# Optimization experiments

Hardware: AMD Instinct MI355X
Metric: run time of the kernel (lower is better)

Reference implementation:

```python
import jax, jax.numpy as jnp
import numpy as np

N = 4096
DIM = 128      # dim_in
HID = 256      # mlp hidden_dim
K_IN = 8       # k for linear_k

def _knn_edges(dist, k):
    # dist: [n,n]; k nearest neighbors excluding self (matches heapq loop)
    n = dist.shape[0]
    d = jnp.where(jnp.eye(n, dtype=bool), jnp.inf, dist)
    nbr = jax.lax.top_k(-d, k)[1]                     # [n,k] indices of k smallest
    src = jnp.repeat(jnp.arange(n), k)                # res[0] = i
    dst = nbr.reshape(-1)                             # res[1] = neighbor
    return src, dst

def _gcn_conv(x, src, dst, W, b):
    # torch_geometric GCNConv: add self loops + symmetric normalization
    n = x.shape[0]
    loop = jnp.arange(n)
    s = jnp.concatenate([src, loop])
    t = jnp.concatenate([dst, loop])
    xw = x @ W
    deg = jax.ops.segment_sum(jnp.ones(s.shape[0], x.dtype), t, num_segments=n)
    dinv = jax.lax.rsqrt(deg)                         # deg >= 1 due to self loops
    norm = dinv[s] * dinv[t]
    out = jax.ops.segment_sum(norm[:, None] * xw[s], t, num_segments=n)
    return out + b

def _gcn(x, src, dst, Wg1, bg1, Wg2, bg2):
    h = jax.nn.relu(_gcn_conv(x, src, dst, Wg1, bg1))
    h = _gcn_conv(h, src, dst, Wg2, bg2)              # dropout is identity in eval
    return jax.nn.log_softmax(h, axis=1)

def _conv2d(x, w, b):
    y = jax.lax.conv_general_dilated(x, w, (1, 1), 'SAME',
        dimension_numbers=('NCHW', 'OIHW', 'NCHW'))
    return y + b.reshape(1, -1, 1, 1)

def setup_inputs():
    key = jax.random.key(0)
    ks = jax.random.split(key, 20)
    f32 = jnp.float32
    def w(k, shape):
        fan = shape[0]
        return (jax.random.uniform(k, shape, f32) * 2 - 1) * (1.0 / np.sqrt(fan))
    return {
        'data_x_1': jax.random.normal(ks[0], (1, N, 4), f32),
        'data_x_2': jax.random.normal(ks[1], (1, N, K_IN, 4), f32),
        'Wk': w(ks[2], (K_IN, 1)),        'bk': jnp.zeros((1,), f32),
        'Wg1': w(ks[3], (8, DIM // 2)),   'bg1': jnp.zeros((DIM // 2,), f32),
        'Wg2': w(ks[4], (DIM // 2, DIM)), 'bg2': jnp.zeros((DIM,), f32),
        'Wq': w(ks[5], (3 * DIM, DIM)),   'bq': jnp.zeros((DIM,), f32),
        'Wkey': w(ks[6], (3 * DIM, DIM)), 'bkey': jnp.zeros((DIM,), f32),
        'Woff': w(ks[7], (4, DIM)),       'boff': jnp.zeros((DIM,), f32),
        'pw': jnp.full((1,), 0.25, f32),
        'Wf1': w(ks[8], (DIM, HID)),      'bf1': jnp.zeros((HID,), f32),
        'Wf2': w(ks[9], (HID, HID)),      'bf2': jnp.zeros((HID,), f32),
        'Wf3': w(ks[10], (HID, 4)),       'bf3': jnp.zeros((4,), f32),
        'Wcy3': w(ks[11], (1, 1, 1, 3)),  'bcy3': jnp.zeros((1,), f32),
        'Wcx3': w(ks[12], (1, 1, 3, 1)),  'bcx3': jnp.zeros((1,), f32),
        'Wcy5': w(ks[13], (1, 1, 1, 5)),  'bcy5': jnp.zeros((1,), f32),
        'Wcx5': w(ks[14], (1, 1, 5, 1)),  'bcx5': jnp.zeros((1,), f32),
        'Wcy9': w(ks[15], (1, 1, 1, 9)),  'bcy9': jnp.zeros((1,), f32),
        'Wcx9': w(ks[16], (1, 1, 9, 1)),  'bcx9': jnp.zeros((1,), f32),
    }

def reference(data_x_1, data_x_2, Wk, bk, Wg1, bg1, Wg2, bg2, Wq, bq, Wkey, bkey,
              Woff, boff, pw, Wf1, bf1, Wf2, bf2, Wf3, bf3,
              Wcy3, bcy3, Wcx3, bcx3, Wcy5, bcy5, Wcx5, bcx5, Wcy9, bcy9, Wcx9, bcx9):
    # linear_k over k dimension: [1,n,k,4] -> transpose -> [1,n,4,k] -> [1,n,4]
    dx2 = jnp.swapaxes(data_x_2, 2, 3)
    dx2_out = (dx2 @ Wk + bk)[..., 0]
    data_x = jnp.concatenate([data_x_1, dx2_out], axis=2)   # [1,n,8]
    Ot = data_x[:, :, 4:]                                   # [1,n,4]

    pos = data_x[:, :, 0:2]
    diff = pos[:, :, None, :] - pos[:, None, :, :]          # [1,n,n,2]
    distances = jnp.linalg.norm(diff, axis=3)               # [1,n,n]
    maxd = jnp.max(distances, axis=2, keepdims=True)
    oushi_atte = 1.0 - distances / maxd                     # [1,n,n]

    x0 = data_x[0]
    dist0 = jax.lax.stop_gradient(distances[0])             # knn on detached dist
    embs = []
    for kk in (3, 5, 9):
        src, dst = _knn_edges(dist0, kk)
        embs.append(_gcn(x0, src, dst, Wg1, bg1, Wg2, bg2)[None])
    embedding = jnp.concatenate(embs, axis=2)               # [1,n,3*DIM]

    query = embedding @ Wq + bq                             # [1,n,DIM]
    key_t = embedding @ Wkey + bkey
    scores = jnp.einsum('bnd,bmd->bnm', query, key_t) / jnp.sqrt(jnp.float32(DIM))
    A = scores / jnp.max(scores, axis=2, keepdims=True)     # [1,n,n]

    A4 = A[None]                                            # [1,1,n,n]
    c3 = _conv2d(A4, Wcy3, bcy3) + _conv2d(A4, Wcx3, bcx3)
    c5 = _conv2d(A4, Wcy5, bcy5) + _conv2d(A4, Wcx5, bcx5)
    c9 = _conv2d(A4, Wcy9, bcy9) + _conv2d(A4, Wcx9, bcx9)

    A_cat = jnp.concatenate([A, oushi_atte, c3[0], c5[0], c9[0]], axis=2)  # [1,n,5n]
    A_cat = (A_cat - A_cat.min()) / (A_cat.max() - A_cat.min())

    Ot5 = jnp.tile(Ot, (1, 5, 1))                           # [1,5n,4]
    h = jnp.matmul(A_cat, Ot5)                              # [1,n,4]
    h = h @ Woff + boff                                     # [1,n,DIM]
    h = jnp.where(h > 0, h, pw * h)                         # PReLU (scalar weight)
    h = jax.nn.relu(h @ Wf1 + bf1)
    h = jax.nn.relu(h @ Wf2 + bf2)
    return h @ Wf3 + bf3                                    # [1,n,4]
```

## Files before the change

### kernel.cpp

```cpp
#include <hip/hip_runtime.h>
#include <math.h>

#define NN 4096

typedef __bf16 bf16x8 __attribute__((ext_vector_type(8)));
typedef float  f32x4  __attribute__((ext_vector_type(4)));

static __device__ __forceinline__ unsigned enc_f(float f){
    unsigned u = __float_as_uint(f);
    return (u & 0x80000000u) ? ~u : (u | 0x80000000u);
}
static __device__ __forceinline__ float dec_f(unsigned u){
    unsigned b = (u & 0x80000000u) ? (u & 0x7fffffffu) : ~u;
    return __uint_as_float(b);
}

__global__ void k_prep(const float* __restrict__ dx1, const float* __restrict__ dx2,
                       const float* __restrict__ Wk, const float* __restrict__ bk,
                       float* __restrict__ x0, float* __restrict__ colsum){
    int n = blockIdx.x*blockDim.x + threadIdx.x;
    if (n >= NN) return;
    float wk[8];
    #pragma unroll
    for (int j=0;j<8;j++) wk[j] = Wk[j];
    float bkv = bk[0];
    #pragma unroll
    for (int c=0;c<4;c++) x0[n*8+c] = dx1[n*4+c];
    #pragma unroll
    for (int c=0;c<4;c++){
        float acc = bkv;
        #pragma unroll
        for (int j=0;j<8;j++) acc += dx2[(n*8+j)*4+c]*wk[j];
        x0[n*8+4+c] = acc;
        atomicAdd(&colsum[c], acc);
    }
}

__global__ void k_ty(const float* __restrict__ x0,
        const float* __restrict__ Wcy3, const float* __restrict__ Wcy5, const float* __restrict__ Wcy9,
        float* __restrict__ Ty){
    int j = blockIdx.x*256 + threadIdx.x;
    if (j >= NN) return;
    float Cy[9];
    #pragma unroll
    for (int o=-4;o<=4;o++){
        float c = Wcy9[o+4];
        if (o>=-2 && o<=2) c += Wcy5[o+2];
        if (o>=-1 && o<=1) c += Wcy3[o+1];
        Cy[o+4] = c;
    }
    float4 acc = {0,0,0,0};
    #pragma unroll
    for (int o=-4;o<=4;o++){
        int jj = j - o;
        if ((unsigned)jj < NN){
            float4 ot = *(const float4*)&x0[jj*8+4];
            float c = Cy[o+4];
            acc.x += c*ot.x; acc.y += c*ot.y; acc.z += c*ot.z; acc.w += c*ot.w;
        }
    }
    *(float4*)&Ty[j*4] = acc;
}

__global__ __launch_bounds__(256) void k_dist(const float* __restrict__ dx1,
        const float* __restrict__ x0,
        float* __restrict__ maxd, int* __restrict__ nbr,
        int* __restrict__ cnt3, int* __restrict__ cnt5, int* __restrict__ cnt9,
        float* __restrict__ dOt){
    __shared__ float2 ps[NN];
    int tid = threadIdx.x;
    for (int j=tid; j<NN; j+=256){
        float4 v = *(const float4*)&dx1[j*4];
        ps[j] = make_float2(v.x, v.y);
    }
    __syncthreads();
    int lane = tid & 63;
    int i = blockIdx.x*4 + (tid>>6);
    float2 pi = ps[i];
    unsigned long long best[9];
    #pragma unroll
    for (int q=0;q<9;q++) best[q] = ~0ULL;
    float lmax = 0.f;
    float4 dacc = {0,0,0,0};
    for (int t=0;t<64;t++){
        int j = (t<<6) | lane;
        float2 p = ps[j];
        float dx = pi.x - p.x, dy = pi.y - p.y;
        float d = sqrtf(dx*dx + dy*dy);
        lmax = fmaxf(lmax, d);
        float4 otj = *(const float4*)&x0[j*8+4];
        dacc.x += d*otj.x; dacc.y += d*otj.y; dacc.z += d*otj.z; dacc.w += d*otj.w;
        unsigned long long cand = ((unsigned long long)__float_as_uint(d) << 32) | (unsigned)j;
        if (j != i && cand < best[8]){
            best[8] = cand;
            #pragma unroll
            for (int q=8; q>0; --q){
                if (best[q] < best[q-1]){ unsigned long long tm=best[q]; best[q]=best[q-1]; best[q-1]=tm; }
            }
        }
    }
    #pragma unroll
    for (int m=1;m<64;m<<=1){
        lmax = fmaxf(lmax, __shfl_xor(lmax, m, 64));
        dacc.x += __shfl_xor(dacc.x, m, 64);
        dacc.y += __shfl_xor(dacc.y, m, 64);
        dacc.z += __shfl_xor(dacc.z, m, 64);
        dacc.w += __shfl_xor(dacc.w, m, 64);
    }
    if (lane==0){
        maxd[i] = lmax;
        *(float4*)&dOt[i*4] = dacc;
    }
    for (int t=0;t<9;t++){
        unsigned long long w = best[0];
        #pragma unroll
        for (int m=1;m<64;m<<=1){
            unsigned long long o = __shfl_xor(w, m, 64);
            if (o < w) w = o;
        }
        if (best[0] == w){
            #pragma unroll
            for (int q=0;q<8;q++) best[q] = best[q+1];
            best[8] = ~0ULL;
        }
        if (lane==0){
            int j = (int)(w & 0xffffffffu);
            nbr[i*9+t] = j;
            atomicAdd(&cnt9[j], 1);
            if (t<5) atomicAdd(&cnt5[j], 1);
            if (t<3) atomicAdd(&cnt3[j], 1);
        }
    }
}

__global__ __launch_bounds__(256) void k_scan(const int* __restrict__ cnt3,
        const int* __restrict__ cnt5, const int* __restrict__ cnt9,
        int* __restrict__ offc, float* __restrict__ dinvc){
    __shared__ int part[256];
    int tid = threadIdx.x;
    for (int g=0; g<3; g++){
        const int* cp = g==0?cnt3:(g==1?cnt5:cnt9);
        int base = tid*16;
        int loc[16]; int s=0;
        #pragma unroll
        for (int q=0;q<16;q++){ loc[q]=s; s += cp[base+q]; }
        part[tid]=s; __syncthreads();
        for (int d=1; d<256; d<<=1){
            int v = (tid>=d) ? part[tid-d] : 0;
            __syncthreads();
            part[tid] += v;
            __syncthreads();
        }
        int pre = (tid==0) ? 0 : part[tid-1];
        #pragma unroll
        for (int q=0;q<16;q++){
            offc[g*NN + base + q]  = pre + loc[q];
            dinvc[g*NN + base + q] = rsqrtf((float)cp[base+q] + 1.f);
        }
        __syncthreads();
    }
}

__global__ void k_fill(const int* __restrict__ nbr, const int* __restrict__ offc,
        int* __restrict__ cur, int* __restrict__ rev){
    int i = blockIdx.x*256 + threadIdx.x;
    if (i >= NN) return;
    #pragma unroll
    for (int t=0;t<9;t++){
        int j = nbr[i*9+t];
        int gmin = t<3 ? 0 : (t<5 ? 1 : 2);
        for (int g=gmin; g<3; g++){
            int pos = atomicAdd(&cur[g*NN+j], 1);
            int rb = (g==0) ? 0 : (g==1 ? NN*3 : NN*8);
            rev[rb + offc[g*NN+j] + pos] = i;
        }
    }
}

__global__ void k_y1(const float* __restrict__ x0, const float* __restrict__ Wg1,
                     float* __restrict__ xw){
    int idx = blockIdx.x*256 + threadIdx.x;
    if (idx >= NN*64) return;
    int n = idx>>6, c = idx&63;
    float acc = 0.f;
    #pragma unroll
    for (int k=0;k<8;k++) acc += x0[n*8+k]*Wg1[k*64+c];
    xw[idx] = acc;
}

__global__ __launch_bounds__(256) void k_h1y2(const float* __restrict__ xw,
        const int* __restrict__ offc,
        const int* __restrict__ cnt3, const int* __restrict__ cnt5, const int* __restrict__ cnt9,
        const int* __restrict__ rev, const float* __restrict__ dinvc,
        const float* __restrict__ bg1, const float* __restrict__ Wg2,
        float* __restrict__ y2){
    __shared__ float h1s[12][64];
    int n0 = blockIdx.x*4, tid = threadIdx.x;
    for (int s=tid; s<768; s+=256){
        int p = s>>6, k = s&63, g = p>>2, n = n0+(p&3);
        const int* cp = g==0?cnt3:(g==1?cnt5:cnt9);
        int rb = (g==0) ? 0 : (g==1 ? NN*3 : NN*8);
        int cnt = cp[n];
        int o = rb + offc[g*NN+n];
        float dv = dinvc[g*NN+n];
        float srow = dv*xw[n*64+k];
        for (int e=0;e<cnt;e++){
            int i = rev[o+e];
            srow += dinvc[g*NN+i]*xw[i*64+k];
        }
        float v = dv*srow + bg1[k];
        h1s[p][k] = v>0.f ? v : 0.f;
    }
    __syncthreads();
    int c = tid & 127, ph = tid>>7;
    float a6[6] = {0,0,0,0,0,0};
    for (int k=0;k<64;k++){
        float w = Wg2[k*128+c];
        #pragma unroll
        for (int q=0;q<6;q++) a6[q] += h1s[q*2+ph][k]*w;
    }
    #pragma unroll
    for (int q=0;q<6;q++){
        int p = q*2+ph, g = p>>2, n = n0+(p&3);
        float dv = dinvc[g*NN+n];
        y2[(size_t)g*NN*128 + (size_t)n*128 + c] = dv*a6[q];
    }
}

__global__ __launch_bounds__(128) void k_fin(const float* __restrict__ y2,
        const int* __restrict__ offc,
        const int* __restrict__ cnt3, const int* __restrict__ cnt5, const int* __restrict__ cnt9,
        const int* __restrict__ rev, const float* __restrict__ dinvc,
        const float* __restrict__ bg2, float* __restrict__ emb){
    __shared__ float sm[2], ss[2];
    int b = blockIdx.x;
    int n = b & (NN-1), g = b >> 12;
    const int* cp = g==0?cnt3:(g==1?cnt5:cnt9);
    int rb = (g==0) ? 0 : (g==1 ? NN*3 : NN*8);
    int cnt = cp[n];
    int o = rb + offc[g*NN+n];
    float dv = dinvc[g*NN+n];
    int c = threadIdx.x;
    const float* yg = y2 + (size_t)g*NN*128;
    float s = yg[(size_t)n*128 + c];
    for (int e=0;e<cnt;e++){
        int i = rev[o+e];
        s += yg[(size_t)i*128 + c];
    }
    float v = dv*s + bg2[c];
    float m = v;
    #pragma unroll
    for (int st=1;st<64;st<<=1) m = fmaxf(m, __shfl_xor(m, st, 64));
    if ((c&63)==0) sm[c>>6] = m;
    __syncthreads();
    m = fmaxf(sm[0], sm[1]);
    float e = expf(v - m);
    float t = e;
    #pragma unroll
    for (int st=1;st<64;st<<=1) t += __shfl_xor(t, st, 64);
    if ((c&63)==0) ss[c>>6] = t;
    __syncthreads();
    t = ss[0]+ss[1];
    emb[n*384 + g*128 + c] = v - m - logf(t);
}

__global__ __launch_bounds__(256) void k_qk(const float* __restrict__ emb,
        const float* __restrict__ Wq, const float* __restrict__ bq,
        const float* __restrict__ Wkey, const float* __restrict__ bkey,
        __bf16* __restrict__ qh, __bf16* __restrict__ ql,
        __bf16* __restrict__ kh, __bf16* __restrict__ kl){
    __shared__ float es[8][384];
    int n0 = blockIdx.x*8;
    int tid = threadIdx.x;
    for (int idx=tid; idx<8*384; idx+=256){
        int m = idx/384, k = idx%384;
        es[m][k] = emb[(n0+m)*384+k];
    }
    __syncthreads();
    int c = tid & 127;
    int sel = tid >> 7;
    const float* W = sel ? Wkey : Wq;
    float b = sel ? bkey[c] : bq[c];
    float acc[8];
    #pragma unroll
    for (int m=0;m<8;m++) acc[m]=b;
    for (int k=0;k<384;k++){
        float w = W[k*128+c];
        #pragma unroll
        for (int m=0;m<8;m++) acc[m] += es[m][k]*w;
    }
    __bf16* oh = sel ? kh : qh;
    __bf16* ol = sel ? kl : ql;
    #pragma unroll
    for (int m=0;m<8;m++){
        float v = acc[m];
        __bf16 h = (__bf16)v;
        oh[(size_t)(n0+m)*128+c] = h;
        ol[(size_t)(n0+m)*128+c] = (__bf16)(v - (float)h);
    }
}

__global__ __launch_bounds__(256) void k_scores(
        const __bf16* __restrict__ qh, const __bf16* __restrict__ ql,
        const __bf16* __restrict__ kh, const __bf16* __restrict__ kl,
        float* __restrict__ scores,
        unsigned* __restrict__ rowmaxenc, unsigned* __restrict__ rowminenc){
    int bx = blockIdx.x & 31;
    int by = blockIdx.x >> 5;
    int tid = threadIdx.x;
    int w = tid >> 6, lane = tid & 63;
    int li = lane & 15, g = lane >> 4;
    int r0 = by*128 + (w>>1)*64;
    int c0 = bx*128 + (w&1)*64;

    f32x4 acc[4][4] = {};
    for (int ks=0; ks<4; ++ks){
        int kofs = ks*32 + g*8;
        bf16x8 ah[4], al[4], bh[4], bl[4];
        #pragma unroll
        for (int f=0; f<4; ++f){
            ah[f] = *(const bf16x8*)&qh[(size_t)(r0+f*16+li)*128 + kofs];
            al[f] = *(const bf16x8*)&ql[(size_t)(r0+f*16+li)*128 + kofs];
            bh[f] = *(const bf16x8*)&kh[(size_t)(c0+f*16+li)*128 + kofs];
            bl[f] = *(const bf16x8*)&kl[(size_t)(c0+f*16+li)*128 + kofs];
        }
        #pragma unroll
        for (int fr=0; fr<4; ++fr){
            #pragma unroll
            for (int fc=0; fc<4; ++fc){
                acc[fr][fc] = __builtin_amdgcn_mfma_f32_16x16x32_bf16(ah[fr], bh[fc], acc[fr][fc], 0, 0, 0);
                acc[fr][fc] = __builtin_amdgcn_mfma_f32_16x16x32_bf16(ah[fr], bl[fc], acc[fr][fc], 0, 0, 0);
                acc[fr][fc] = __builtin_amdgcn_mfma_f32_16x16x32_bf16(al[fr], bh[fc], acc[fr][fc], 0, 0, 0);
            }
        }
    }
    #pragma unroll
    for (int fr=0; fr<4; ++fr){
        #pragma unroll
        for (int r=0; r<4; ++r){
            int row = r0 + fr*16 + g*4 + r;
            float mx = -INFINITY, mn = INFINITY;
            #pragma unroll
            for (int fc=0; fc<4; ++fc){
                float v = acc[fr][fc][r];
                scores[(size_t)row*NN + c0 + fc*16 + li] = v;
                mx = fmaxf(mx, v);
                mn = fminf(mn, v);
            }
            #pragma unroll
            for (int s=1; s<16; s<<=1){
                mx = fmaxf(mx, __shfl_xor(mx, s, 64));
                mn = fminf(mn, __shfl_xor(mn, s, 64));
            }
            if (li == 0){
                atomicMax(&rowmaxenc[row], enc_f(mx));
                atomicMin(&rowminenc[row], enc_f(mn));
            }
        }
    }
}

__global__ __launch_bounds__(256) void k_cstream(const float* __restrict__ scores,
        const unsigned* __restrict__ rowmaxenc,
        const float* __restrict__ Wcy3, const float* __restrict__ Wcx3,
        const float* __restrict__ Wcy5, const float* __restrict__ Wcx5,
        const float* __restrict__ Wcy9, const float* __restrict__ Wcx9,
        const float* __restrict__ bcy3, const float* __restrict__ bcx3,
        const float* __restrict__ bcy5, const float* __restrict__ bcx5,
        const float* __restrict__ bcy9, const float* __restrict__ bcx9,
        float* __restrict__ mnmx){
    __shared__ float smn[4], smx[4];
    int tid = threadIdx.x;
    int w = tid >> 6, lane = tid & 63;
    int strip = blockIdx.x*4 + w;
    int jj = strip*56 - 4 + lane;
    bool cvalid = (unsigned)jj < NN;
    bool outLane = (lane >= 4) && (lane < 60) && cvalid;
    int i0 = blockIdx.y*64;

    float wy3[3],wx3[3],wy5[5],wx5[5],wy9[9],wx9[9];
    #pragma unroll
    for (int t=0;t<3;t++){ wy3[t]=Wcy3[t]; wx3[t]=Wcx3[t]; }
    #pragma unroll
    for (int t=0;t<5;t++){ wy5[t]=Wcy5[t]; wx5[t]=Wcx5[t]; }
    #pragma unroll
    for (int t=0;t<9;t++){ wy9[t]=Wcy9[t]; wx9[t]=Wcx9[t]; }
    float bc3 = bcy3[0]+bcx3[0];
    float bc5 = bcy5[0]+bcx5[0];
    float bc9 = bcy9[0]+bcx9[0];

    float win[9], cy3r[9], cy5r[9], cy9r[9];
    float mn = INFINITY, mx = -INFINITY;

    for (int tb = 0; tb < 8; ++tb){
        #pragma unroll
        for (int u = 0; u < 9; ++u){
            int t  = tb*9 + u;
            int ri = i0 - 4 + t;
            float a = 0.f;
            if (((unsigned)ri < NN) && cvalid)
                a = scores[(size_t)ri*NN + jj] * (1.f/dec_f(rowmaxenc[ri]));
            float tp[9];
            #pragma unroll
            for (int k=0;k<9;k++) tp[k] = (k==4) ? a : __shfl(a, lane + k - 4, 64);
            float cy9v = ((tp[0]*wy9[0] + tp[1]*wy9[1]) + (tp[2]*wy9[2] + tp[3]*wy9[3]))
                       + ((tp[4]*wy9[4] + tp[5]*wy9[5]) + (tp[6]*wy9[6] + tp[7]*wy9[7]))
                       + tp[8]*wy9[8];
            float cy5v = ((tp[2]*wy5[0] + tp[3]*wy5[1]) + (tp[4]*wy5[2] + tp[5]*wy5[3]))
                       + tp[6]*wy5[4];
            float cy3v = (tp[3]*wy3[0] + tp[4]*wy3[1]) + tp[5]*wy3[2];
            win[u]  = a;
            cy3r[u] = cy3v; cy5r[u] = cy5v; cy9r[u] = cy9v;
            if (t >= 8 && outLane){
                float cx9v = ((win[(u+1)%9]*wx9[0] + win[(u+2)%9]*wx9[1]) + (win[(u+3)%9]*wx9[2] + win[(u+4)%9]*wx9[3]))
                           + ((win[(u+5)%9]*wx9[4] + win[(u+6)%9]*wx9[5]) + (win[(u+7)%9]*wx9[6] + win[(u+8)%9]*wx9[7]))
                           + win[u]*wx9[8];
                float cx5v = ((win[(u+3)%9]*wx5[0] + win[(u+4)%9]*wx5[1]) + (win[(u+5)%9]*wx5[2] + win[(u+6)%9]*wx5[3]))
                           + win[(u+7)%9]*wx5[4];
                float cx3v = (win[(u+4)%9]*wx3[0] + win[(u+5)%9]*wx3[1]) + win[(u+6)%9]*wx3[2];
                float c9 = cy9r[(u+5)%9] + cx9v + bc9;
                float c5 = cy5r[(u+5)%9] + cx5v + bc5;
                float c3 = cy3r[(u+5)%9] + cx3v + bc3;
                mn = fminf(mn, fminf(fminf(c3,c5),c9));
                mx = fmaxf(mx, fmaxf(fmaxf(c3,c5),c9));
            }
        }
    }
    #pragma unroll
    for (int m=1; m<64; m<<=1){
        mn = fminf(mn, __shfl_xor(mn, m, 64));
        mx = fmaxf(mx, __shfl_xor(mx, m, 64));
    }
    if (lane == 0){ smn[w] = mn; smx[w] = mx; }
    __syncthreads();
    if (tid == 0){
        float a0 = fminf(fminf(smn[0],smn[1]), fminf(smn[2],smn[3]));
        float b0 = fmaxf(fmaxf(smx[0],smx[1]), fmaxf(smx[2],smx[3]));
        int bid = blockIdx.y*gridDim.x + blockIdx.x;
        mnmx[bid] = a0;
        mnmx[1216 + bid] = b0;
    }
}

__global__ __launch_bounds__(256) void k_rowdot(const float* __restrict__ scores,
        const float* __restrict__ x0, const float* __restrict__ Ty,
        const unsigned* __restrict__ rowmaxenc, const float* __restrict__ maxd,
        const float* __restrict__ dOt, const float* __restrict__ colsum,
        const float* __restrict__ bcy3, const float* __restrict__ bcx3,
        const float* __restrict__ bcy5, const float* __restrict__ bcx5,
        const float* __restrict__ bcy9, const float* __restrict__ bcx9,
        float* __restrict__ ASdot, float* __restrict__ Bv){
    int tid = threadIdx.x;
    int tc = tid & 31, tr = tid >> 5;
    int i = blockIdx.x*8 + tr;
    const float* srow = scores + (size_t)i*NN;
    float4 ss = {0,0,0,0}, st = {0,0,0,0};
    for (int c0 = tc; c0 < NN; c0 += 32){
        float sv = srow[c0];
        float4 ot = *(const float4*)&x0[c0*8+4];
        float4 ty = *(const float4*)&Ty[c0*4];
        ss.x += sv*ot.x; ss.y += sv*ot.y; ss.z += sv*ot.z; ss.w += sv*ot.w;
        st.x += sv*ty.x; st.y += sv*ty.y; st.z += sv*ty.z; st.w += sv*ty.w;
    }
    #pragma unroll
    for (int s=1; s<32; s<<=1){
        ss.x += __shfl_xor(ss.x, s, 64); ss.y += __shfl_xor(ss.y, s, 64);
        ss.z += __shfl_xor(ss.z, s, 64); ss.w += __shfl_xor(ss.w, s, 64);
        st.x += __shfl_xor(st.x, s, 64); st.y += __shfl_xor(st.y, s, 64);
        st.z += __shfl_xor(st.z, s, 64); st.w += __shfl_xor(st.w, s, 64);
    }
    if (tc == 0){
        float iv = 1.f/dec_f(rowmaxenc[i]);
        float imv = 1.f/maxd[i];
        float bcsum = bcy3[0]+bcx3[0]+bcy5[0]+bcx5[0]+bcy9[0]+bcx9[0];
        float4 cs = *(const float4*)colsum;
        float4 dv = *(const float4*)&dOt[i*4];
        float4 as;
        as.x = iv*ss.x; as.y = iv*ss.y; as.z = iv*ss.z; as.w = iv*ss.w;
        float k = 1.f + bcsum;
        float4 b;
        b.x = cs.x*k - imv*dv.x + iv*st.x;
        b.y = cs.y*k - imv*dv.y + iv*st.y;
        b.z = cs.z*k - imv*dv.z + iv*st.z;
        b.w = cs.w*k - imv*dv.w + iv*st.w;
        *(float4*)&ASdot[i*4] = as;
        *(float4*)&Bv[i*4]   = b;
    }
}

__global__ __launch_bounds__(256) void k_gmm(const float* __restrict__ mnmx,
        const unsigned* __restrict__ rowminenc, const unsigned* __restrict__ rowmaxenc,
        float* __restrict__ gmm){
    __shared__ float smn[256], smx[256];
    int tid = threadIdx.x;
    float mn = 0.f, mx = 1.f;
    for (int i=tid; i<NN; i+=256){
        float rmx = dec_f(rowmaxenc[i]);
        float q = dec_f(rowminenc[i]) / rmx;
        mn = fminf(mn, fminf(1.f, q));
        mx = fmaxf(mx, fmaxf(1.f, q));
    }
    for (int b=tid; b<1216; b+=256){
        mn = fminf(mn, mnmx[b]);
        mx = fmaxf(mx, mnmx[1216+b]);
    }
    smn[tid]=mn; smx[tid]=mx; __syncthreads();
    for (int s=128;s>0;s>>=1){
        if (tid<s){ smn[tid]=fminf(smn[tid],smn[tid+s]); smx[tid]=fmaxf(smx[tid],smx[tid+s]); }
        __syncthreads();
    }
    if (tid==0){ gmm[0]=smn[0]; gmm[1]=smx[0]; }
}

__global__ void k_hfin(const float* __restrict__ ASdot, const float* __restrict__ Bv,
        const float* __restrict__ Wcx3, const float* __restrict__ Wcx5, const float* __restrict__ Wcx9,
        const float* __restrict__ gmm, const float* __restrict__ colsum,
        float* __restrict__ hfin){
    int i = blockIdx.x*256 + threadIdx.x;
    if (i >= NN) return;
    float Cx[9];
    #pragma unroll
    for (int o=-4;o<=4;o++){
        float c = Wcx9[o+4];
        if (o>=-2 && o<=2) c += Wcx5[o+2];
        if (o>=-1 && o<=1) c += Wcx3[o+1];
        Cx[o+4] = c;
    }
    float4 h = *(const float4*)&Bv[i*4];
    float4 a0 = *(const float4*)&ASdot[i*4];
    h.x += a0.x; h.y += a0.y; h.z += a0.z; h.w += a0.w;
    #pragma unroll
    for (int o=-4;o<=4;o++){
        int r = i + o;
        if ((unsigned)r < NN){
            float4 av = *(const float4*)&ASdot[r*4];
            float c = Cx[o+4];
            h.x += c*av.x; h.y += c*av.y; h.z += c*av.z; h.w += c*av.w;
        }
    }
    float mnv = gmm[0], mxv = gmm[1];
    float s = 1.f/(mxv-mnv), oa = -mnv*s;
    float4 cs = *(const float4*)colsum;
    float4 out;
    out.x = s*h.x + 5.f*oa*cs.x;
    out.y = s*h.y + 5.f*oa*cs.y;
    out.z = s*h.z + 5.f*oa*cs.z;
    out.w = s*h.w + 5.f*oa*cs.w;
    *(float4*)&hfin[i*4] = out;
}

__global__ __launch_bounds__(256) void k_mlp(const float* __restrict__ hfin,
        const float* __restrict__ Woff, const float* __restrict__ boff, const float* __restrict__ pw,
        const float* __restrict__ Wf1, const float* __restrict__ bf1,
        const float* __restrict__ Wf2, const float* __restrict__ bf2,
        const float* __restrict__ Wf3, const float* __restrict__ bf3,
        float* __restrict__ out){
    __shared__ float h1[8][128];
    __shared__ float h2[8][256];
    __shared__ float h3[8][256];
    __shared__ float4 red4[256];
    int n0 = blockIdx.x*8, tid = threadIdx.x;
    float p = pw[0];
    {
        int c = tid & 127, mb = (tid>>7)*4;
        #pragma unroll
        for (int mm=0; mm<4; mm++){
            int m = mb+mm;
            float v = boff[c];
            #pragma unroll
            for (int k=0;k<4;k++) v += hfin[(n0+m)*4+k]*Woff[k*128+c];
            h1[m][c] = v>0.f ? v : p*v;
        }
    }
    __syncthreads();
    {
        int c = tid;
        float acc[8];
        #pragma unroll
        for (int m=0;m<8;m++) acc[m] = bf1[c];
        for (int k=0;k<128;k++){
            float w = Wf1[k*256+c];
            #pragma unroll
            for (int m=0;m<8;m++) acc[m] += h1[m][k]*w;
        }
        #pragma unroll
        for (int m=0;m<8;m++) h2[m][c] = acc[m]>0.f?acc[m]:0.f;
    }
    __syncthreads();
    {
        int c = tid;
        float acc[8];
        #pragma unroll
        for (int m=0;m<8;m++) acc[m] = bf2[c];
        for (int k=0;k<256;k++){
            float w = Wf2[k*256+c];
            #pragma unroll
            for (int m=0;m<8;m++) acc[m] += h2[m][k]*w;
        }
        #pragma unroll
        for (int m=0;m<8;m++) h3[m][c] = acc[m]>0.f?acc[m]:0.f;
    }
    __syncthreads();
    float w3_0 = Wf3[tid*4+0], w3_1 = Wf3[tid*4+1], w3_2 = Wf3[tid*4+2], w3_3 = Wf3[tid*4+3];
    for (int m=0;m<8;m++){
        float hv = h3[m][tid];
        float4 r; r.x = hv*w3_0; r.y = hv*w3_1; r.z = hv*w3_2; r.w = hv*w3_3;
        red4[tid]=r; __syncthreads();
        for (int s=128;s>0;s>>=1){
            if(tid<s){
                red4[tid].x+=red4[tid+s].x; red4[tid].y+=red4[tid+s].y;
                red4[tid].z+=red4[tid+s].z; red4[tid].w+=red4[tid+s].w;
            }
            __syncthreads();
        }
        if (tid==0){
            float4 o;
            o.x = red4[0].x + bf3[0]; o.y = red4[0].y + bf3[1];
            o.z = red4[0].z + bf3[2]; o.w = red4[0].w + bf3[3];
            *(float4*)&out[(n0+m)*4] = o;
        }
        __syncthreads();
    }
}

extern "C" void kernel_launch(void* const* d_in, const int* in_sizes, int n_in,
                              void* d_out, int out_size, void* d_ws, size_t ws_size,
                              hipStream_t stream){
    const float* dx1  = (const float*)d_in[0];
    const float* dx2  = (const float*)d_in[1];
    const float* Wk   = (const float*)d_in[2];
    const float* bk   = (const float*)d_in[3];
    const float* Wg1  = (const float*)d_in[4];
    const float* bg1  = (const float*)d_in[5];
    const float* Wg2  = (const float*)d_in[6];
    const float* bg2  = (const float*)d_in[7];
    const float* Wq   = (const float*)d_in[8];
    const float* bq   = (const float*)d_in[9];
    const float* Wkey = (const float*)d_in[10];
    const float* bkey = (const float*)d_in[11];
    const float* Woff = (const float*)d_in[12];
    const float* boff = (const float*)d_in[13];
    const float* pw   = (const float*)d_in[14];
    const float* Wf1  = (const float*)d_in[15];
    const float* bf1  = (const float*)d_in[16];
    const float* Wf2  = (const float*)d_in[17];
    const float* bf2  = (const float*)d_in[18];
    const float* Wf3  = (const float*)d_in[19];
    const float* bf3  = (const float*)d_in[20];
    const float* Wcy3 = (const float*)d_in[21];
    const float* bcy3 = (const float*)d_in[22];
    const float* Wcx3 = (const float*)d_in[23];
    const float* bcx3 = (const float*)d_in[24];
    const float* Wcy5 = (const float*)d_in[25];
    const float* bcy5 = (const float*)d_in[26];
    const float* Wcx5 = (const float*)d_in[27];
    const float* bcx5 = (const float*)d_in[28];
    const float* Wcy9 = (const float*)d_in[29];
    const float* bcy9 = (const float*)d_in[30];
    const float* Wcx9 = (const float*)d_in[31];
    const float* bcx9 = (const float*)d_in[32];

    char* ws = (char*)d_ws;
    size_t off = 0;
    auto alloc = [&](size_t b)->void*{ void* p = ws + off; off += (b + 255) & ~(size_t)255; return p; };

    char* zbase = ws + off;
    float*    colsum    = (float*)   alloc(4*4);
    int*      cnt3      = (int*)     alloc((size_t)NN*4);
    int*      cnt5      = (int*)     alloc((size_t)NN*4);
    int*      cnt9      = (int*)     alloc((size_t)NN*4);
    int*      cur       = (int*)     alloc((size_t)3*NN*4);
    unsigned* rowmaxenc = (unsigned*)alloc((size_t)NN*4);
    size_t zbytes = (size_t)((ws + off) - zbase);
    unsigned* rowminenc = (unsigned*)alloc((size_t)NN*4);

    float* x0     = (float*)alloc((size_t)NN*8*4);
    float* maxd   = (float*)alloc((size_t)NN*4);
    int*   nbr    = (int*)  alloc((size_t)NN*9*4);
    int*   offc   = (int*)  alloc((size_t)3*NN*4);
    float* dinvc  = (float*)alloc((size_t)3*NN*4);
    int*   rev    = (int*)  alloc((size_t)NN*17*4);
    float* xw     = (float*)alloc((size_t)NN*64*4);
    float* y2     = (float*)alloc((size_t)3*NN*128*4);
    float* emb    = (float*)alloc((size_t)NN*384*4);
    __bf16* qh   = (__bf16*)alloc((size_t)NN*128*2);
    __bf16* ql   = (__bf16*)alloc((size_t)NN*128*2);
    __bf16* kh   = (__bf16*)alloc((size_t)NN*128*2);
    __bf16* kl   = (__bf16*)alloc((size_t)NN*128*2);
    float* scores = (float*)alloc((size_t)NN*NN*4);
    float* Tyb    = (float*)alloc((size_t)NN*4*4);
    float* dOt    = (float*)alloc((size_t)NN*4*4);
    float* ASd    = (float*)alloc((size_t)NN*4*4);
    float* Bv     = (float*)alloc((size_t)NN*4*4);
    float* mnmx   = (float*)alloc((size_t)2*1216*4);
    float* gmm    = (float*)alloc(2*4);
    float* hfin   = (float*)alloc((size_t)NN*4*4);
    (void)ws_size; (void)in_sizes; (void)n_in; (void)out_size;

    hipMemsetAsync(zbase, 0, zbytes, stream);
    hipMemsetAsync(rowminenc, 0xFF, (size_t)NN*4, stream);

    k_prep<<<16,256,0,stream>>>(dx1,dx2,Wk,bk,x0,colsum);
    k_ty  <<<16,256,0,stream>>>(x0,Wcy3,Wcy5,Wcy9,Tyb);
    k_dist<<<NN/4,256,0,stream>>>(dx1,x0,maxd,nbr,cnt3,cnt5,cnt9,dOt);
    k_scan<<<1,256,0,stream>>>(cnt3,cnt5,cnt9,offc,dinvc);
    k_fill<<<16,256,0,stream>>>(nbr,offc,cur,rev);

    k_y1  <<<NN*64/256,256,0,stream>>>(x0,Wg1,xw);
    k_h1y2<<<NN/4,256,0,stream>>>(xw,offc,cnt3,cnt5,cnt9,rev,dinvc,bg1,Wg2,y2);
    k_fin <<<NN*3,128,0,stream>>>(y2,offc,cnt3,cnt5,cnt9,rev,dinvc,bg2,emb);

    k_qk<<<NN/8,256,0,stream>>>(emb,Wq,bq,Wkey,bkey,qh,ql,kh,kl);
    k_scores<<<1024,256,0,stream>>>(qh,ql,kh,kl,scores,rowmaxenc,rowminenc);

    k_cstream<<<dim3(19,64),256,0,stream>>>(scores,rowmaxenc,
        Wcy3,Wcx3,Wcy5,Wcx5,Wcy9,Wcx9,
        bcy3,bcx3,bcy5,bcx5,bcy9,bcx9, mnmx);
    k_rowdot<<<NN/8,256,0,stream>>>(scores,x0,Tyb,rowmaxenc,maxd,dOt,colsum,
        bcy3,bcx3,bcy5,bcx5,bcy9,bcx9, ASd, Bv);
    k_gmm<<<1,256,0,stream>>>(mnmx,rowminenc,rowmaxenc,gmm);
    k_hfin<<<16,256,0,stream>>>(ASd,Bv,Wcx3,Wcx5,Wcx9,gmm,colsum,hfin);
    k_mlp<<<NN/8,256,0,stream>>>(hfin,Woff,boff,pw,Wf1,bf1,Wf2,bf2,Wf3,bf3,(float*)d_out);
}
```

Before: 347.2 us.

## Fuse conv-stream min/max pass with row dot products over scores

Merges the conv stencil min/max sweep and the row-dot pass over the 64MB scores matrix into one kernel, so scores is read once instead of twice. Each lane now handles four contiguous columns through float4 loads, and row-direction neighbours come from lane shuffles. Per-strip partial dot products go to a new buffer that a small reduction kernel sums. Row max inverses are precomputed in their own kernel. The cost is a full 64-lane shuffle reduction for every output row, a larger partial buffer, and extra launches.

```diff
diff --git a/kernel.cpp b/kernel.cpp
--- a/kernel.cpp
+++ b/kernel.cpp
@@ -13,6 +13,14 @@
 static __device__ __forceinline__ float dec_f(unsigned u){
     unsigned b = (u & 0x80000000u) ? (u & 0x7fffffffu) : ~u;
     return __uint_as_float(b);
+}
+static __device__ __forceinline__ float4 shfl4(float4 v, int src){
+    float4 r;
+    r.x = __shfl(v.x, src, 64);
+    r.y = __shfl(v.y, src, 64);
+    r.z = __shfl(v.z, src, 64);
+    r.w = __shfl(v.w, src, 64);
+    return r;
 }
 
 __global__ void k_prep(const float* __restrict__ dx1, const float* __restrict__ dx2,
@@ -360,23 +368,31 @@
     }
 }
 
-__global__ __launch_bounds__(256) void k_cstream(const float* __restrict__ scores,
-        const unsigned* __restrict__ rowmaxenc,
+__global__ void k_invr(const unsigned* __restrict__ rowmaxenc, float* __restrict__ invr){
+    int i = blockIdx.x*256 + threadIdx.x;
+    if (i >= NN) return;
+    invr[i] = 1.f/dec_f(rowmaxenc[i]);
+}
+
+__global__ __launch_bounds__(256) void k_cfuse(const float* __restrict__ scores,
+        const float* __restrict__ invr,
+        const float* __restrict__ x0, const float* __restrict__ Ty,
         const float* __restrict__ Wcy3, const float* __restrict__ Wcx3,
         const float* __restrict__ Wcy5, const float* __restrict__ Wcx5,
         const float* __restrict__ Wcy9, const float* __restrict__ Wcx9,
         const float* __restrict__ bcy3, const float* __restrict__ bcx3,
         const float* __restrict__ bcy5, const float* __restrict__ bcx5,
         const float* __restrict__ bcy9, const float* __restrict__ bcx9,
-        float* __restrict__ mnmx){
+        float* __restrict__ mnmx, float* __restrict__ hpart){
     __shared__ float smn[4], smx[4];
     int tid = threadIdx.x;
     int w = tid >> 6, lane = tid & 63;
-    int strip = blockIdx.x*4 + w;
-    int jj = strip*56 - 4 + lane;
-    bool cvalid = (unsigned)jj < NN;
-    bool outLane = (lane >= 4) && (lane < 60) && cvalid;
-    int i0 = blockIdx.y*64;
+    int strip = blockIdx.x;
+    int rb = blockIdx.y*4 + w;
+    int i0 = rb*28;
+    int colbase = strip*248 - 4 + lane*4;
+    bool lv = (colbase >= 0) && (colbase + 3 < NN);
+    bool outLane = (lane >= 1) && (lane < 63) && lv;
 
     float wy3[3],wx3[3],wy5[5],wx5[5],wy9[9],wx9[9];
     #pragma unroll
@@ -389,40 +405,76 @@
     float bc5 = bcy5[0]+bcx5[0];
     float bc9 = bcy9[0]+bcx9[0];
 
-    float win[9], cy3r[9], cy5r[9], cy9r[9];
+    float4 ot[4], ty[4];
+    #pragma unroll
+    for (int c=0;c<4;c++){
+        if (lv){
+            ot[c] = *(const float4*)&x0[(colbase+c)*8+4];
+            ty[c] = *(const float4*)&Ty[(colbase+c)*4];
+        } else {
+            ot[c] = make_float4(0,0,0,0);
+            ty[c] = make_float4(0,0,0,0);
+        }
+    }
+
+    float4 win[9];
     float mn = INFINITY, mx = -INFINITY;
-
-    for (int tb = 0; tb < 8; ++tb){
+    const int laneL = lane - 1, laneR = lane + 1;
+
+    for (int tb = 0; tb < 4; ++tb){
         #pragma unroll
         for (int u = 0; u < 9; ++u){
             int t  = tb*9 + u;
             int ri = i0 - 4 + t;
-            float a = 0.f;
-            if (((unsigned)ri < NN) && cvalid)
-                a = scores[(size_t)ri*NN + jj] * (1.f/dec_f(rowmaxenc[ri]));
-            float tp[9];
-            #pragma unroll
-            for (int k=0;k<9;k++) tp[k] = (k==4) ? a : __shfl(a, lane + k - 4, 64);
-            float cy9v = ((tp[0]*wy9[0] + tp[1]*wy9[1]) + (tp[2]*wy9[2] + tp[3]*wy9[3]))
-                       + ((tp[4]*wy9[4] + tp[5]*wy9[5]) + (tp[6]*wy9[6] + tp[7]*wy9[7]))
-                       + tp[8]*wy9[8];
-            float cy5v = ((tp[2]*wy5[0] + tp[3]*wy5[1]) + (tp[4]*wy5[2] + tp[5]*wy5[3]))
-                       + tp[6]*wy5[4];
-            float cy3v = (tp[3]*wy3[0] + tp[4]*wy3[1]) + tp[5]*wy3[2];
-            win[u]  = a;
-            cy3r[u] = cy3v; cy5r[u] = cy5v; cy9r[u] = cy9v;
-            if (t >= 8 && outLane){
-                float cx9v = ((win[(u+1)%9]*wx9[0] + win[(u+2)%9]*wx9[1]) + (win[(u+3)%9]*wx9[2] + win[(u+4)%9]*wx9[3]))
-                           + ((win[(u+5)%9]*wx9[4] + win[(u+6)%9]*wx9[5]) + (win[(u+7)%9]*wx9[6] + win[(u+8)%9]*wx9[7]))
-                           + win[u]*wx9[8];
-                float cx5v = ((win[(u+3)%9]*wx5[0] + win[(u+4)%9]*wx5[1]) + (win[(u+5)%9]*wx5[2] + win[(u+6)%9]*wx5[3]))
-                           + win[(u+7)%9]*wx5[4];
-                float cx3v = (win[(u+4)%9]*wx3[0] + win[(u+5)%9]*wx3[1]) + win[(u+6)%9]*wx3[2];
-                float c9 = cy9r[(u+5)%9] + cx9v + bc9;
-                float c5 = cy5r[(u+5)%9] + cx5v + bc5;
-                float c3 = cy3r[(u+5)%9] + cx3v + bc3;
-                mn = fminf(mn, fminf(fminf(c3,c5),c9));
-                mx = fmaxf(mx, fmaxf(fmaxf(c3,c5),c9));
+            float4 a = make_float4(0,0,0,0);
+            if (((unsigned)ri < NN) && lv){
+                float iv = invr[ri];
+                float4 v = *(const float4*)&scores[(size_t)ri*NN + colbase];
+                a.x = v.x*iv; a.y = v.y*iv; a.z = v.z*iv; a.w = v.w*iv;
+            }
+            win[u] = a;
+            int ro = i0 + t - 8;
+            if (t >= 8 && ro < NN){
+                float4 ctr = win[(u+5)%9];
+                float4 wl = shfl4(ctr, laneL);
+                float4 wr = shfl4(ctr, laneR);
+                float cw[12] = {wl.x,wl.y,wl.z,wl.w, ctr.x,ctr.y,ctr.z,ctr.w, wr.x,wr.y,wr.z,wr.w};
+                float4 pA = make_float4(0,0,0,0), pT = make_float4(0,0,0,0);
+                if (outLane){
+                    #pragma unroll
+                    for (int c=0;c<4;c++){
+                        float cx9 = ((win[(u+1)%9][c]*wx9[0] + win[(u+2)%9][c]*wx9[1]) + (win[(u+3)%9][c]*wx9[2] + win[(u+4)%9][c]*wx9[3]))
+                                  + ((win[(u+5)%9][c]*wx9[4] + win[(u+6)%9][c]*wx9[5]) + (win[(u+7)%9][c]*wx9[6] + win[(u+8)%9][c]*wx9[7]))
+                                  + win[u][c]*wx9[8];
+                        float cx5 = ((win[(u+3)%9][c]*wx5[0] + win[(u+4)%9][c]*wx5[1]) + (win[(u+5)%9][c]*wx5[2] + win[(u+6)%9][c]*wx5[3]))
+                                  + win[(u+7)%9][c]*wx5[4];
+                        float cx3 = (win[(u+4)%9][c]*wx3[0] + win[(u+5)%9][c]*wx3[1]) + win[(u+6)%9][c]*wx3[2];
+                        float cy9 = ((cw[c+0]*wy9[0] + cw[c+1]*wy9[1]) + (cw[c+2]*wy9[2] + cw[c+3]*wy9[3]))
+                                  + ((cw[c+4]*wy9[4] + cw[c+5]*wy9[5]) + (cw[c+6]*wy9[6] + cw[c+7]*wy9[7]))
+                                  + cw[c+8]*wy9[8];
+                        float cy5 = ((cw[c+2]*wy5[0] + cw[c+3]*wy5[1]) + (cw[c+4]*wy5[2] + cw[c+5]*wy5[3]))
+                                  + cw[c+6]*wy5[4];
+                        float cy3 = (cw[c+3]*wy3[0] + cw[c+4]*wy3[1]) + cw[c+5]*wy3[2];
+                        float c3v = cy3+cx3+bc3, c5v = cy5+cx5+bc5, c9v = cy9+cx9+bc9;
+                        mn = fminf(mn, fminf(fminf(c3v,c5v),c9v));
+                        mx = fmaxf(mx, fmaxf(fmaxf(c3v,c5v),c9v));
+                        float av = cw[c+4];
+                        pA.x += av*ot[c].x; pA.y += av*ot[c].y; pA.z += av*ot[c].z; pA.w += av*ot[c].w;
+                        pT.x += av*ty[c].x; pT.y += av*ty[c].y; pT.z += av*ty[c].z; pT.w += av*ty[c].w;
+                    }
+                }
+                #pragma unroll
+                for (int m=1; m<64; m<<=1){
+                    pA.x += __shfl_xor(pA.x, m, 64); pA.y += __shfl_xor(pA.y, m, 64);
+                    pA.z += __shfl_xor(pA.z, m, 64); pA.w += __shfl_xor(pA.w, m, 64);
+                    pT.x += __shfl_xor(pT.x, m, 64); pT.y += __shfl_xor(pT.y, m, 64);
+                    pT.z += __shfl_xor(pT.z, m, 64); pT.w += __shfl_xor(pT.w, m, 64);
+                }
+                if (lane == 0){
+                    float* hp = &hpart[((size_t)ro*17 + strip)*8];
+                    *(float4*)hp = pA;
+                    *(float4*)(hp+4) = pT;
+                }
             }
         }
     }
@@ -438,53 +490,7 @@
         float b0 = fmaxf(fmaxf(smx[0],smx[1]), fmaxf(smx[2],smx[3]));
         int bid = blockIdx.y*gridDim.x + blockIdx.x;
         mnmx[bid] = a0;
-        mnmx[1216 + bid] = b0;
-    }
-}
-
-__global__ __launch_bounds__(256) void k_rowdot(const float* __restrict__ scores,
-        const float* __restrict__ x0, const float* __restrict__ Ty,
-        const unsigned* __restrict__ rowmaxenc, const float* __restrict__ maxd,
-        const float* __restrict__ dOt, const float* __restrict__ colsum,
-        const float* __restrict__ bcy3, const float* __restrict__ bcx3,
-        const float* __restrict__ bcy5, const float* __restrict__ bcx5,
-        const float* __restrict__ bcy9, const float* __restrict__ bcx9,
-        float* __restrict__ ASdot, float* __restrict__ Bv){
-    int tid = threadIdx.x;
-    int tc = tid & 31, tr = tid >> 5;
-    int i = blockIdx.x*8 + tr;
-    const float* srow = scores + (size_t)i*NN;
-    float4 ss = {0,0,0,0}, st = {0,0,0,0};
-    for (int c0 = tc; c0 < NN; c0 += 32){
-        float sv = srow[c0];
-        float4 ot = *(const float4*)&x0[c0*8+4];
-        float4 ty = *(const float4*)&Ty[c0*4];
-        ss.x += sv*ot.x; ss.y += sv*ot.y; ss.z += sv*ot.z; ss.w += sv*ot.w;
-        st.x += sv*ty.x; st.y += sv*ty.y; st.z += sv*ty.z; st.w += sv*ty.w;
-    }
-    #pragma unroll
-    for (int s=1; s<32; s<<=1){
-        ss.x += __shfl_xor(ss.x, s, 64); ss.y += __shfl_xor(ss.y, s, 64);
-        ss.z += __shfl_xor(ss.z, s, 64); ss.w += __shfl_xor(ss.w, s, 64);
-        st.x += __shfl_xor(st.x, s, 64); st.y += __shfl_xor(st.y, s, 64);
-        st.z += __shfl_xor(st.z, s, 64); st.w += __shfl_xor(st.w, s, 64);
-    }
-    if (tc == 0){
-        float iv = 1.f/dec_f(rowmaxenc[i]);
-        float imv = 1.f/maxd[i];
-        float bcsum = bcy3[0]+bcx3[0]+bcy5[0]+bcx5[0]+bcy9[0]+bcx9[0];
-        float4 cs = *(const float4*)colsum;
-        float4 dv = *(const float4*)&dOt[i*4];
-        float4 as;
-        as.x = iv*ss.x; as.y = iv*ss.y; as.z = iv*ss.z; as.w = iv*ss.w;
-        float k = 1.f + bcsum;
-        float4 b;
-        b.x = cs.x*k - imv*dv.x + iv*st.x;
-        b.y = cs.y*k - imv*dv.y + iv*st.y;
-        b.z = cs.z*k - imv*dv.z + iv*st.z;
-        b.w = cs.w*k - imv*dv.w + iv*st.w;
-        *(float4*)&ASdot[i*4] = as;
-        *(float4*)&Bv[i*4]   = b;
+        mnmx[640 + bid] = b0;
     }
 }
 
@@ -500,9 +506,9 @@
         mn = fminf(mn, fminf(1.f, q));
         mx = fmaxf(mx, fmaxf(1.f, q));
     }
-    for (int b=tid; b<1216; b+=256){
+    for (int b=tid; b<629; b+=256){
         mn = fminf(mn, mnmx[b]);
-        mx = fmaxf(mx, mnmx[1216+b]);
+        mx = fmaxf(mx, mnmx[640+b]);
     }
     smn[tid]=mn; smx[tid]=mx; __syncthreads();
     for (int s=128;s>0;s>>=1){
@@ -510,6 +516,38 @@
         __syncthreads();
     }
     if (tid==0){ gmm[0]=smn[0]; gmm[1]=smx[0]; }
+}
+
+__global__ void k_hred(const float* __restrict__ hpart,
+        const float* __restrict__ maxd, const float* __restrict__ dOt,
+        const float* __restrict__ colsum,
+        const float* __restrict__ bcy3, const float* __restrict__ bcx3,
+        const float* __restrict__ bcy5, const float* __restrict__ bcx5,
+        const float* __restrict__ bcy9, const float* __restrict__ bcx9,
+        float* __restrict__ ASdot, float* __restrict__ Bv){
+    int i = blockIdx.x*256 + threadIdx.x;
+    if (i >= NN) return;
+    float4 pa = {0,0,0,0}, pt = {0,0,0,0};
+    const float* hp = &hpart[(size_t)i*17*8];
+    #pragma unroll
+    for (int s=0; s<17; ++s){
+        float4 a = *(const float4*)&hp[s*8];
+        float4 t = *(const float4*)&hp[s*8+4];
+        pa.x+=a.x; pa.y+=a.y; pa.z+=a.z; pa.w+=a.w;
+        pt.x+=t.x; pt.y+=t.y; pt.z+=t.z; pt.w+=t.w;
+    }
+    float imv = 1.f/maxd[i];
+    float bcsum = bcy3[0]+bcx3[0]+bcy5[0]+bcx5[0]+bcy9[0]+bcx9[0];
+    float k = 1.f + bcsum;
+    float4 cs = *(const float4*)colsum;
+    float4 dv = *(const float4*)&dOt[i*4];
+    float4 b;
+    b.x = cs.x*k - imv*dv.x + pt.x;
+    b.y = cs.y*k - imv*dv.y + pt.y;
+    b.z = cs.z*k - imv*dv.z + pt.z;
+    b.w = cs.w*k - imv*dv.w + pt.w;
+    *(float4*)&ASdot[i*4] = pa;
+    *(float4*)&Bv[i*4]    = b;
 }
 
 __global__ void k_hfin(const float* __restrict__ ASdot, const float* __restrict__ Bv,
@@ -689,10 +727,12 @@
     __bf16* kl   = (__bf16*)alloc((size_t)NN*128*2);
     float* scores = (float*)alloc((size_t)NN*NN*4);
     float* Tyb    = (float*)alloc((size_t)NN*4*4);
+    float* invr   = (float*)alloc((size_t)NN*4);
     float* dOt    = (float*)alloc((size_t)NN*4*4);
     float* ASd    = (float*)alloc((size_t)NN*4*4);
     float* Bv     = (float*)alloc((size_t)NN*4*4);
-    float* mnmx   = (float*)alloc((size_t)2*1216*4);
+    float* hpart  = (float*)alloc((size_t)NN*17*8*4);
+    float* mnmx   = (float*)alloc((size_t)2*640*4);
     float* gmm    = (float*)alloc(2*4);
     float* hfin   = (float*)alloc((size_t)NN*4*4);
     (void)ws_size; (void)in_sizes; (void)n_in; (void)out_size;
@@ -712,13 +752,14 @@
 
     k_qk<<<NN/8,256,0,stream>>>(emb,Wq,bq,Wkey,bkey,qh,ql,kh,kl);
     k_scores<<<1024,256,0,stream>>>(qh,ql,kh,kl,scores,rowmaxenc,rowminenc);
-
-    k_cstream<<<dim3(19,64),256,0,stream>>>(scores,rowmaxenc,
+    k_invr<<<16,256,0,stream>>>(rowmaxenc,invr);
+
+    k_cfuse<<<dim3(17,37),256,0,stream>>>(scores,invr,x0,Tyb,
         Wcy3,Wcx3,Wcy5,Wcx5,Wcy9,Wcx9,
-        bcy3,bcx3,bcy5,bcx5,bcy9,bcx9, mnmx);
-    k_rowdot<<<NN/8,256,0,stream>>>(scores,x0,Tyb,rowmaxenc,maxd,dOt,colsum,
+        bcy3,bcx3,bcy5,bcx5,bcy9,bcx9, mnmx, hpart);
+    k_gmm<<<1,256,0,stream>>>(mnmx,rowminenc,rowmaxenc,gmm);
+    k_hred<<<16,256,0,stream>>>(hpart,maxd,dOt,colsum,
         bcy3,bcx3,bcy5,bcx5,bcy9,bcx9, ASd, Bv);
-    k_gmm<<<1,256,0,stream>>>(mnmx,rowminenc,rowmaxenc,gmm);
     k_hfin<<<16,256,0,stream>>>(ASd,Bv,Wcx3,Wcx5,Wcx9,gmm,colsum,hfin);
     k_mlp<<<NN/8,256,0,stream>>>(hfin,Woff,boff,pw,Wf1,bf1,Wf2,bf2,Wf3,bf3,(float*)d_out);
 }
```

After: 334.5 us. 3.7% less time.
